# Performance work log

Measured on AMD Instinct MI355X. Metric: run time of the kernel, lower is better.

## Reference

```python
import jax, jax.numpy as jnp
import numpy as np
from jax import lax

W = 50      # window size
EPS = 1e-5  # BatchNorm eps (torch default)


def setup_inputs() -> dict:
    key = jax.random.key(0)
    ks = jax.random.split(key, 40)
    def n(i, shape, s=0.1):
        return (jax.random.normal(ks[i], shape, dtype=jnp.float32) * s).astype(jnp.float32)
    inp = {}
    inp['x'] = jax.random.normal(ks[0], (16, 1, 2048), dtype=jnp.float32)
    # conv stack (eval-mode BatchNorm: running mean/var are params)
    inp['conv1_w'] = n(1, (64, 1, 9));  inp['conv1_b'] = n(2, (64,))
    inp['bn1_g'] = 1.0 + n(3, (64,));   inp['bn1_b'] = n(4, (64,))
    inp['bn1_m'] = n(5, (64,));         inp['bn1_v'] = 0.5 + jax.random.uniform(ks[6], (64,), dtype=jnp.float32)
    inp['conv2_w'] = n(7, (32, 64, 7)); inp['conv2_b'] = n(8, (32,))
    inp['bn2_g'] = 1.0 + n(9, (32,));   inp['bn2_b'] = n(10, (32,))
    inp['bn2_m'] = n(11, (32,));        inp['bn2_v'] = 0.5 + jax.random.uniform(ks[12], (32,), dtype=jnp.float32)
    inp['conv3_w'] = n(13, (16, 32, 5)); inp['conv3_b'] = n(14, (16,))
    inp['bn3_g'] = 1.0 + n(15, (16,));   inp['bn3_b'] = n(16, (16,))
    inp['bn3_m'] = n(17, (16,));         inp['bn3_v'] = 0.5 + jax.random.uniform(ks[18], (16,), dtype=jnp.float32)
    # 2-layer LSTM, hidden 64, input 16 (torch gate order i,f,g,o)
    H = 64
    inp['wih0'] = n(19, (4 * H, 16)); inp['whh0'] = n(20, (4 * H, H))
    inp['bih0'] = n(21, (4 * H,));    inp['bhh0'] = n(22, (4 * H,))
    inp['wih1'] = n(23, (4 * H, H));  inp['whh1'] = n(24, (4 * H, H))
    inp['bih1'] = n(25, (4 * H,));    inp['bhh1'] = n(26, (4 * H,))
    # classifier 64 -> 32 -> 2
    inp['fc1_w'] = n(27, (32, H)); inp['fc1_b'] = n(28, (32,))
    inp['fc2_w'] = n(29, (2, 32)); inp['fc2_b'] = n(30, (2,))
    return inp


def _conv1d(x, w, b, pad):
    # x: [N, Cin, L], w: [Cout, Cin, K]
    y = lax.conv_general_dilated(x, w, (1,), [(pad, pad)],
                                 dimension_numbers=('NCH', 'OIH', 'NCH'))
    return y + b[:, None]


def _bn(x, g, b, m, v):
    # eval-mode BatchNorm1d over channel dim of [N, C, L]
    return (x - m[:, None]) * (g / jnp.sqrt(v + EPS))[:, None] + b[:, None]


def _lstm_layer(x, wih, whh, bih, bhh):
    # x: [B, T, D] -> [B, T, H]; torch gate order (i, f, g, o)
    B, T, D = x.shape
    H = whh.shape[1]
    xs = jnp.transpose(x, (1, 0, 2))                     # [T, B, D]
    pre = xs @ wih.T + (bih + bhh)                       # [T, B, 4H] input projection, hoisted
    def step(carry, p):
        h, c = carry
        g = p + h @ whh.T
        i, f, gg, o = jnp.split(g, 4, axis=-1)
        c = jax.nn.sigmoid(f) * c + jax.nn.sigmoid(i) * jnp.tanh(gg)
        h = jax.nn.sigmoid(o) * jnp.tanh(c)
        return (h, c), h
    h0 = jnp.zeros((B, H), x.dtype)
    _, hs = lax.scan(step, (h0, h0), pre)
    return jnp.transpose(hs, (1, 0, 2))


def reference(x, conv1_w, conv1_b, bn1_g, bn1_b, bn1_m, bn1_v,
              conv2_w, conv2_b, bn2_g, bn2_b, bn2_m, bn2_v,
              conv3_w, conv3_b, bn3_g, bn3_b, bn3_m, bn3_v,
              wih0, whh0, bih0, bhh0, wih1, whh1, bih1, bhh1,
              fc1_w, fc1_b, fc2_w, fc2_b):
    B, C, T = x.shape
    # sliding windows with left zero-pad of W-1 -> [B, T, C, W]
    xp = jnp.pad(x, ((0, 0), (0, 0), (W - 1, 0)))
    idx = jnp.arange(T)[:, None] + jnp.arange(W)[None, :]  # [T, W]
    win = xp[:, :, idx]                                    # [B, C, T, W]
    win = jnp.transpose(win, (0, 2, 1, 3)).reshape(B * T, C, W)
    # conv -> BN(eval) -> ReLU stack (dropout is identity in eval)
    h = jax.nn.relu(_bn(_conv1d(win, conv1_w, conv1_b, 4), bn1_g, bn1_b, bn1_m, bn1_v))
    h = jax.nn.relu(_bn(_conv1d(h, conv2_w, conv2_b, 3), bn2_g, bn2_b, bn2_m, bn2_v))
    h = jax.nn.relu(_bn(_conv1d(h, conv3_w, conv3_b, 2), bn3_g, bn3_b, bn3_m, bn3_v))
    feats = h.mean(axis=-1).reshape(B, T, -1)              # AdaptiveAvgPool1d(1) -> [B, T, 16]
    # 2-layer LSTM
    h1 = _lstm_layer(feats, wih0, whh0, bih0, bhh0)
    h2 = _lstm_layer(h1, wih1, whh1, bih1, bhh1)           # [B, T, 64]
    # classifier
    z = jax.nn.relu(h2 @ fc1_w.T + fc1_b)
    logits = z @ fc2_w.T + fc2_b                           # [B, T, 2]
    return logits
```

## Files before the change

### kernel.cpp

```cpp
#include <hip/hip_runtime.h>

#define EPSV 1e-5f
#define SCOPE_AGENT __HIP_MEMORY_SCOPE_AGENT

__device__ __forceinline__ float fast_rcp(float x) { return __builtin_amdgcn_rcpf(x); }
__device__ __forceinline__ float tanhfast(float x) {
    float e = __expf(2.0f * x);
    return 1.0f - 2.0f * fast_rcp(e + 1.0f);
}
__device__ __forceinline__ float dot4(const float4 w, const float4 v, float a) {
    a = fmaf(w.x, v.x, a);
    a = fmaf(w.y, v.y, a);
    a = fmaf(w.z, v.z, a);
    a = fmaf(w.w, v.w, a);
    return a;
}
#define DPPF(v, ctrl) __int_as_float(__builtin_amdgcn_mov_dpp(__float_as_int(v), (ctrl), 0xF, 0xF, false))

typedef unsigned long long ull;

struct RecS {
    float hbuf[2][80];
    float ring[16][64];
    float xst[16][80];
};
struct EdgeS {
    float A1[64 * 36];
    float A2[32 * 36];
    float xl[16], xr[16];
    float s1[64], t1[64], s2[32], t2[32], s3[16], t3[16];
    float psumE[288];
    float pi[512];
};

__global__ void pack_kernel(const float* __restrict__ w2, const float* __restrict__ w3,
                            float* __restrict__ w2t2, float4* __restrict__ w3p4,
                            float* __restrict__ w3p1, int* __restrict__ sync_ints) {
    int j = blockIdx.x * 256 + threadIdx.x;
    if (j < 16384) {
        int i = j >> 8;
        int o = (j >> 3) & 31;
        int k = j & 7;
        w2t2[j] = (k < 7) ? w2[o * 448 + i * 7 + k] : 0.0f;
    } else if (j < 16896) {
        int e = j - 16384;
        int i = e >> 4, o = e & 15;
        int base = o * 160 + i * 5;
        w3p4[e] = make_float4(w3[base], w3[base + 1], w3[base + 2], w3[base + 3]);
        w3p1[e] = w3[base + 4];
    } else if (j < 16896 + 4096) {
        sync_ints[j - 16896] = 0;
    }
}

__global__ __launch_bounds__(256) void conv1f_kernel(
    const float* __restrict__ x, const float* __restrict__ w1,
    const float* __restrict__ b1, const float* __restrict__ g1,
    const float* __restrict__ be1, const float* __restrict__ m1,
    const float* __restrict__ vv1, float* __restrict__ a1f)
{
    __shared__ float xs[72];
    const int tid = threadIdx.x;
    const int T = blockIdx.x * 64;
    const int b = blockIdx.y;
    if (tid < 72) {
        int gi = T - 49 + tid;
        xs[tid] = (gi >= 0 && gi < 2048) ? x[b * 2048 + gi] : 0.0f;
    }
    const int i = tid & 63, q = tid >> 6;
    float wv[9];
    #pragma unroll
    for (int k = 0; k < 9; ++k) wv[k] = w1[i * 9 + k];
    float sc = g1[i] * rsqrtf(vv1[i] + EPSV);
    float tc = (b1[i] - m1[i]) * sc + be1[i];
    __syncthreads();
    #pragma unroll
    for (int r = 0; r < 16; ++r) {
        int v1 = T + q * 16 + r;
        if (v1 < 2089) {
            float acc = 0.0f;
            #pragma unroll
            for (int k = 0; k < 9; ++k) acc = fmaf(wv[k], xs[q * 16 + r + k], acc);
            a1f[((long)b * 2089 + v1) * 64 + i] = fmaxf(acc * sc + tc, 0.0f);
        }
    }
}

__global__ __launch_bounds__(256) void conv2f_kernel(
    const float* __restrict__ a1f, const float* __restrict__ w2t2,
    const float* __restrict__ b2, const float* __restrict__ g2,
    const float* __restrict__ be2, const float* __restrict__ m2,
    const float* __restrict__ vv2, float* __restrict__ a2f)
{
    __shared__ __align__(16) float As[64 * 104];
    const int tid = threadIdx.x;
    const int T = blockIdx.x * 64;
    const int b = blockIdx.y;
    for (int idx = tid; idx < 1120; idx += 256) {
        int j = idx >> 4, i4 = (idx & 15) * 4;
        int v1 = T + j; if (v1 > 2088) v1 = 2088;
        float4 f = *(const float4*)&a1f[((long)b * 2089 + v1) * 64 + i4];
        int sj = j + ((j >> 3) << 2);
        As[(i4 + 0) * 104 + sj] = f.x;
        As[(i4 + 1) * 104 + sj] = f.y;
        As[(i4 + 2) * 104 + sj] = f.z;
        As[(i4 + 3) * 104 + sj] = f.w;
    }
    const int o = tid >> 3, pg = tid & 7;
    float sc = g2[o] * rsqrtf(vv2[o] + EPSV);
    float tc = (b2[o] - m2[o]) * sc + be2[o];
    __syncthreads();
    float acc[8];
    #pragma unroll
    for (int q = 0; q < 8; ++q) acc[q] = 0.0f;
    for (int i = 0; i < 64; ++i) {
        const float* rowp = &As[i * 104 + 12 * pg];
        float4 A0 = *(const float4*)&rowp[0];
        float4 A1 = *(const float4*)&rowp[4];
        float4 A2 = *(const float4*)&rowp[12];
        float2 A3 = *(const float2*)&rowp[16];
        const float4* wp = (const float4*)&w2t2[(i * 32 + o) * 8];
        float4 Wa = wp[0], Wb = wp[1];
        float av[14] = {A0.x, A0.y, A0.z, A0.w, A1.x, A1.y, A1.z, A1.w,
                        A2.x, A2.y, A2.z, A2.w, A3.x, A3.y};
        float wk[7] = {Wa.x, Wa.y, Wa.z, Wa.w, Wb.x, Wb.y, Wb.z};
        #pragma unroll
        for (int k = 0; k < 7; ++k) {
            #pragma unroll
            for (int q = 0; q < 8; ++q) acc[q] = fmaf(wk[k], av[q + k], acc[q]);
        }
    }
    #pragma unroll
    for (int q = 0; q < 8; ++q) {
        int v2 = T + pg * 8 + q;
        if (v2 < 2083)
            a2f[((long)b * 2083 + v2) * 32 + o] = fmaxf(acc[q] * sc + tc, 0.0f);
    }
}

__global__ __launch_bounds__(256) void conv3f_kernel(
    const float* __restrict__ a2f,
    const float4* __restrict__ w3p4, const float* __restrict__ w3p1,
    const float* __restrict__ b3, const float* __restrict__ g3,
    const float* __restrict__ be3, const float* __restrict__ m3,
    const float* __restrict__ vv3, float* __restrict__ a3f)
{
    __shared__ __align__(16) float A2s[32 * 200];
    const int tid = threadIdx.x;
    const int T = blockIdx.x * 128;
    const int b = blockIdx.y;
    for (int idx = tid; idx < 1056; idx += 256) {
        int j = idx >> 3, i4 = (idx & 7) * 4;
        int v2 = T + j; if (v2 > 2082) v2 = 2082;
        float4 f = *(const float4*)&a2f[((long)b * 2083 + v2) * 32 + i4];
        int sj = j + ((j >> 3) << 2);
        A2s[(i4 + 0) * 200 + sj] = f.x;
        A2s[(i4 + 1) * 200 + sj] = f.y;
        A2s[(i4 + 2) * 200 + sj] = f.z;
        A2s[(i4 + 3) * 200 + sj] = f.w;
    }
    const int o = tid & 15, pg = tid >> 4;
    float sc = g3[o] * rsqrtf(vv3[o] + EPSV);
    float tc = (b3[o] - m3[o]) * sc + be3[o];
    __syncthreads();
    float acc[8];
    #pragma unroll
    for (int q = 0; q < 8; ++q) acc[q] = 0.0f;
    for (int i = 0; i < 32; ++i) {
        const float* rowp = &A2s[i * 200 + 12 * pg];
        float4 R0 = *(const float4*)&rowp[0];
        float4 R1 = *(const float4*)&rowp[4];
        float4 R2 = *(const float4*)&rowp[12];
        float av[12] = {R0.x, R0.y, R0.z, R0.w, R1.x, R1.y, R1.z, R1.w,
                        R2.x, R2.y, R2.z, R2.w};
        float4 wa = w3p4[i * 16 + o];
        float w4 = w3p1[i * 16 + o];
        #pragma unroll
        for (int q = 0; q < 8; ++q) {
            acc[q] = fmaf(wa.x, av[q], acc[q]);
            acc[q] = fmaf(wa.y, av[q + 1], acc[q]);
            acc[q] = fmaf(wa.z, av[q + 2], acc[q]);
            acc[q] = fmaf(wa.w, av[q + 3], acc[q]);
            acc[q] = fmaf(w4,   av[q + 4], acc[q]);
        }
    }
    #pragma unroll
    for (int q = 0; q < 8; ++q) {
        int v3 = T + pg * 8 + q;
        if (v3 < 2079)
            a3f[((long)b * 2080 + v3) * 16 + o] = fmaxf(acc[q] * sc + tc, 0.0f);
        else if (v3 < 2080)
            a3f[((long)b * 2080 + v3) * 16 + o] = 0.0f;
    }
}

__device__ __forceinline__ void rec0_body(char* smemraw, int b,
    const float* __restrict__ feats,
    const float* __restrict__ wih, const float* __restrict__ whh,
    const float* __restrict__ bih, const float* __restrict__ bhh,
    float* __restrict__ hout, int* __restrict__ cnt0, int* __restrict__ flag1)
{
    RecS* s = (RecS*)smemraw;
    const int tid = threadIdx.x;
    const int j = tid >> 2, kq = tid & 3;
    __builtin_amdgcn_s_setprio(1);

    const float4* pa = (const float4*)(whh + (0 * 64 + j) * 64 + kq * 16);
    const float4* pb = (const float4*)(whh + (1 * 64 + j) * 64 + kq * 16);
    const float4* pc_ = (const float4*)(whh + (2 * 64 + j) * 64 + kq * 16);
    const float4* pd = (const float4*)(whh + (3 * 64 + j) * 64 + kq * 16);
    float4 A0 = pa[0], A1 = pa[1], A2 = pa[2], A3 = pa[3];
    float4 B0 = pb[0], B1 = pb[1], B2 = pb[2], B3 = pb[3];
    float4 C0 = pc_[0], C1 = pc_[1], C2 = pc_[2], C3 = pc_[3];
    float4 D0 = pd[0], D1 = pd[1], D2 = pd[2], D3 = pd[3];
    float4 xw0 = *(const float4*)(wih + (0 * 64 + j) * 16 + kq * 4);
    float4 xw1 = *(const float4*)(wih + (1 * 64 + j) * 16 + kq * 4);
    float4 xw2 = *(const float4*)(wih + (2 * 64 + j) * 16 + kq * 4);
    float4 xw3 = *(const float4*)(wih + (3 * 64 + j) * 16 + kq * 4);
    const float bb0 = bih[j] + bhh[j];
    const float bb1 = bih[64 + j] + bhh[64 + j];
    const float bb2 = bih[128 + j] + bhh[128 + j];
    const float bb3 = bih[192 + j] + bhh[192 + j];

    if (tid < 64) s->hbuf[1][(tid >> 4) * 20 + (tid & 15)] = 0.0f;
    float cst = 0.0f;
    const float* fbase = feats + (long)b * 32768;
    __syncthreads();

#define STEP0(k) { \
        const float4* hp_ = (const float4*)&s->hbuf[((k) + 1) & 1][kq * 20]; \
        float4 h0_ = hp_[0], h1_ = hp_[1], h2_ = hp_[2], h3_ = hp_[3]; \
        float4 xv_ = *(const float4*)&s->xst[(k)][kq * 4]; \
        float p0 = dot4(A3, h3_, dot4(A2, h2_, dot4(A1, h1_, dot4(A0, h0_, dot4(xw0, xv_, 0.f))))); \
        float p1 = dot4(B3, h3_, dot4(B2, h2_, dot4(B1, h1_, dot4(B0, h0_, dot4(xw1, xv_, 0.f))))); \
        float p2 = dot4(C3, h3_, dot4(C2, h2_, dot4(C1, h1_, dot4(C0, h0_, dot4(xw2, xv_, 0.f))))); \
        float p3 = dot4(D3, h3_, dot4(D2, h2_, dot4(D1, h1_, dot4(D0, h0_, dot4(xw3, xv_, 0.f))))); \
        p0 += DPPF(p0, 0xB1); p1 += DPPF(p1, 0xB1); p2 += DPPF(p2, 0xB1); p3 += DPPF(p3, 0xB1); \
        p0 += DPPF(p0, 0x4E); p1 += DPPF(p1, 0x4E); p2 += DPPF(p2, 0x4E); p3 += DPPF(p3, 0x4E); \
        float gi = 1.0f - fast_rcp(__expf(p0 + bb0) + 1.0f); \
        float gf = 1.0f - fast_rcp(__expf(p1 + bb1) + 1.0f); \
        float gg = 1.0f - 2.0f * fast_rcp(__expf(2.0f * (p2 + bb2)) + 1.0f); \
        float go = 1.0f - fast_rcp(__expf(p3 + bb3) + 1.0f); \
        cst = fmaf(gf, cst, gi * gg); \
        float h_ = go * tanhfast(cst); \
        if (kq == 0) { s->hbuf[(k) & 1][(j >> 4) * 20 + (j & 15)] = h_; s->ring[(k)][j] = h_; } \
        __syncthreads(); \
    }

    for (int c = 0; c < 128; ++c) {
        if (tid == 0) {
            while (__hip_atomic_load(&cnt0[b * 128 + c], __ATOMIC_RELAXED, SCOPE_AGENT) < 16)
                __builtin_amdgcn_s_sleep(2);
        }
        __syncthreads();
        s->xst[tid >> 4][tid & 15] =
            __hip_atomic_load(fbase + c * 256 + tid, __ATOMIC_RELAXED, SCOPE_AGENT);
        __syncthreads();
        STEP0(0)  STEP0(1)  STEP0(2)  STEP0(3)
        STEP0(4)  STEP0(5)  STEP0(6)  STEP0(7)
        STEP0(8)  STEP0(9)  STEP0(10) STEP0(11)
        STEP0(12) STEP0(13) STEP0(14) STEP0(15)
        {
            ull* dst = (ull*)(hout + ((long)b * 2048 + c * 16) * 64);
            ull v0 = ((const ull*)s->ring)[tid];
            ull v1 = ((const ull*)s->ring)[tid + 256];
            __hip_atomic_store(dst + tid, v0, __ATOMIC_RELAXED, SCOPE_AGENT);
            __hip_atomic_store(dst + tid + 256, v1, __ATOMIC_RELAXED, SCOPE_AGENT);
            __syncthreads();
            if (tid == 0)
                __hip_atomic_store(&flag1[b * 128 + c], 1, __ATOMIC_RELAXED, SCOPE_AGENT);
        }
    }
#undef STEP0
}

__device__ __forceinline__ void rec1_body(char* smemraw, int b,
    const float* __restrict__ h1o,
    const float* __restrict__ wih, const float* __restrict__ whh,
    const float* __restrict__ bih, const float* __restrict__ bhh,
    float* __restrict__ hout, int* __restrict__ flag1)
{
    RecS* s = (RecS*)smemraw;
    const int tid = threadIdx.x;
    const int j = tid >> 2, kq = tid & 3;
    __builtin_amdgcn_s_setprio(1);

    const float4* pa = (const float4*)(whh + (0 * 64 + j) * 64 + kq * 16);
    const float4* pb = (const float4*)(whh + (1 * 64 + j) * 64 + kq * 16);
    const float4* pc_ = (const float4*)(whh + (2 * 64 + j) * 64 + kq * 16);
    const float4* pd = (const float4*)(whh + (3 * 64 + j) * 64 + kq * 16);
    float4 A0 = pa[0], A1 = pa[1], A2 = pa[2], A3 = pa[3];
    float4 B0 = pb[0], B1 = pb[1], B2 = pb[2], B3 = pb[3];
    float4 C0 = pc_[0], C1 = pc_[1], C2 = pc_[2], C3 = pc_[3];
    float4 D0 = pd[0], D1 = pd[1], D2 = pd[2], D3 = pd[3];
    const float4* qa = (const float4*)(wih + (0 * 64 + j) * 64 + kq * 16);
    const float4* qb = (const float4*)(wih + (1 * 64 + j) * 64 + kq * 16);
    const float4* qc = (const float4*)(wih + (2 * 64 + j) * 64 + kq * 16);
    const float4* qd = (const float4*)(wih + (3 * 64 + j) * 64 + kq * 16);
    float4 XA0 = qa[0], XA1 = qa[1], XA2 = qa[2], XA3 = qa[3];
    float4 XB0 = qb[0], XB1 = qb[1], XB2 = qb[2], XB3 = qb[3];
    float4 XC0 = qc[0], XC1 = qc[1], XC2 = qc[2], XC3 = qc[3];
    float4 XD0 = qd[0], XD1 = qd[1], XD2 = qd[2], XD3 = qd[3];
    const float bb0 = bih[j] + bhh[j];
    const float bb1 = bih[64 + j] + bhh[64 + j];
    const float bb2 = bih[128 + j] + bhh[128 + j];
    const float bb3 = bih[192 + j] + bhh[192 + j];

    if (tid < 64) s->hbuf[1][(tid >> 4) * 20 + (tid & 15)] = 0.0f;
    float cst = 0.0f;
    __syncthreads();

#define STEP1(k) { \
        const float4* hp_ = (const float4*)&s->hbuf[((k) + 1) & 1][kq * 20]; \
        float4 h0_ = hp_[0], h1_ = hp_[1], h2_ = hp_[2], h3_ = hp_[3]; \
        const float4* xp_ = (const float4*)&s->xst[(k)][kq * 20]; \
        float4 x0_ = xp_[0], x1_ = xp_[1], x2_ = xp_[2], x3_ = xp_[3]; \
        float p0 = dot4(A3, h3_, dot4(A2, h2_, dot4(A1, h1_, dot4(A0, h0_, \
                   dot4(XA3, x3_, dot4(XA2, x2_, dot4(XA1, x1_, dot4(XA0, x0_, 0.f)))))))); \
        float p1 = dot4(B3, h3_, dot4(B2, h2_, dot4(B1, h1_, dot4(B0, h0_, \
                   dot4(XB3, x3_, dot4(XB2, x2_, dot4(XB1, x1_, dot4(XB0, x0_, 0.f)))))))); \
        float p2 = dot4(C3, h3_, dot4(C2, h2_, dot4(C1, h1_, dot4(C0, h0_, \
                   dot4(XC3, x3_, dot4(XC2, x2_, dot4(XC1, x1_, dot4(XC0, x0_, 0.f)))))))); \
        float p3 = dot4(D3, h3_, dot4(D2, h2_, dot4(D1, h1_, dot4(D0, h0_, \
                   dot4(XD3, x3_, dot4(XD2, x2_, dot4(XD1, x1_, dot4(XD0, x0_, 0.f)))))))); \
        p0 += DPPF(p0, 0xB1); p1 += DPPF(p1, 0xB1); p2 += DPPF(p2, 0xB1); p3 += DPPF(p3, 0xB1); \
        p0 += DPPF(p0, 0x4E); p1 += DPPF(p1, 0x4E); p2 += DPPF(p2, 0x4E); p3 += DPPF(p3, 0x4E); \
        float gi = 1.0f - fast_rcp(__expf(p0 + bb0) + 1.0f); \
        float gf = 1.0f - fast_rcp(__expf(p1 + bb1) + 1.0f); \
        float gg = 1.0f - 2.0f * fast_rcp(__expf(2.0f * (p2 + bb2)) + 1.0f); \
        float go = 1.0f - fast_rcp(__expf(p3 + bb3) + 1.0f); \
        cst = fmaf(gf, cst, gi * gg); \
        float h_ = go * tanhfast(cst); \
        if (kq == 0) { s->hbuf[(k) & 1][(j >> 4) * 20 + (j & 15)] = h_; s->ring[(k)][j] = h_; } \
        __syncthreads(); \
    }

    for (int c = 0; c < 128; ++c) {
        if (tid == 0) {
            while (__hip_atomic_load(&flag1[b * 128 + c], __ATOMIC_RELAXED, SCOPE_AGENT) < 1)
                __builtin_amdgcn_s_sleep(2);
        }
        __syncthreads();
        {
            const ull* src = (const ull*)(h1o + ((long)b * 2048 + c * 16) * 64);
            ull v0 = __hip_atomic_load(src + tid, __ATOMIC_RELAXED, SCOPE_AGENT);
            ull v1 = __hip_atomic_load(src + tid + 256, __ATOMIC_RELAXED, SCOPE_AGENT);
            int u0 = tid, u1 = tid + 256;
            int k0 = u0 >> 5, p0i = (u0 & 31) * 2;
            int k1 = u1 >> 5, p1i = (u1 & 31) * 2;
            *(ull*)&s->xst[k0][(p0i >> 4) * 20 + (p0i & 15)] = v0;
            *(ull*)&s->xst[k1][(p1i >> 4) * 20 + (p1i & 15)] = v1;
        }
        __syncthreads();
        STEP1(0)  STEP1(1)  STEP1(2)  STEP1(3)
        STEP1(4)  STEP1(5)  STEP1(6)  STEP1(7)
        STEP1(8)  STEP1(9)  STEP1(10) STEP1(11)
        STEP1(12) STEP1(13) STEP1(14) STEP1(15)
        {
            float4* dst = (float4*)(hout + ((long)b * 2048 + c * 16) * 64);
            dst[tid] = ((const float4*)s->ring)[tid];
        }
    }
#undef STEP1
}

__device__ void edge_worker(char* smemraw, int w,
    const float* __restrict__ x,
    const float* __restrict__ w1,
    const float* __restrict__ b1, const float* __restrict__ g1,
    const float* __restrict__ be1, const float* __restrict__ m1, const float* __restrict__ vv1,
    const float* __restrict__ b2, const float* __restrict__ g2,
    const float* __restrict__ be2, const float* __restrict__ m2, const float* __restrict__ vv2,
    const float* __restrict__ b3, const float* __restrict__ g3,
    const float* __restrict__ be3, const float* __restrict__ m3, const float* __restrict__ vv3,
    const float* __restrict__ w2t2,
    const float4* __restrict__ w3p4, const float* __restrict__ w3p1,
    const float* __restrict__ a1f, const float* __restrict__ a2f,
    const float* __restrict__ a3f,
    float* __restrict__ feats, int* __restrict__ cnt0)
{
    EdgeS* s = (EdgeS*)smemraw;
    const int tid = threadIdx.x;

    for (int idx = tid; idx < 1088; idx += 256) {
        if (idx < 768) {
            int row = idx / 12, z = idx - row * 12;
            int slot = (z < 3) ? z : (z < 6 ? 10 + z : 20 + z);
            s->A1[row * 36 + slot] = 0.0f;
        } else {
            int e = idx - 768;
            int row = e / 10, z = e - row * 10;
            int slot = (z < 2) ? z : (z < 5 ? 11 + z : 22 + z);
            s->A2[row * 36 + slot] = 0.0f;
        }
    }
    if (tid < 64) {
        float sc = g1[tid] * rsqrtf(vv1[tid] + EPSV);
        s->s1[tid] = sc;
        s->t1[tid] = (b1[tid] - m1[tid]) * sc + be1[tid];
    } else if (tid < 96) {
        int o = tid - 64;
        float sc = g2[o] * rsqrtf(vv2[o] + EPSV);
        s->s2[o] = sc;
        s->t2[o] = (b2[o] - m2[o]) * sc + be2[o];
    } else if (tid < 112) {
        int o = tid - 96;
        float sc = g3[o] * rsqrtf(vv3[o] + EPSV);
        s->s3[o] = sc;
        s->t3[o] = (b3[o] - m3[o]) * sc + be3[o];
    }
    const int o1 = tid >> 2, g1q = tid & 3;
    float wv[9];
    #pragma unroll
    for (int k = 0; k < 9; ++k) wv[k] = w1[o1 * 9 + k];
    __syncthreads();
    const float sc1 = s->s1[o1], tc1 = s->t1[o1];

    for (int tile = w; tile < 32768; tile += 448) {
        const int b = tile & 15, t = tile >> 4;

        if (tid < 128) {
            int dv = tid >> 2, o4 = (tid & 3) * 4;
            *(float4*)&s->pi[dv * 16 + o4] =
                *(const float4*)&a3f[((long)b * 2080 + t + dv) * 16 + o4];
        }
        if (tid >= 112 && tid < 128) {
            int m = tid - 112;
            float v = 0.0f;
            if (m >= 4) { int gi = t - 53 + m; if (gi >= 0) v = x[b * 2048 + gi]; }
            s->xl[m] = v;
        } else if (tid >= 128 && tid < 144) {
            int m = tid - 128;
            float v = 0.0f;
            if (m <= 7) { int gi = t - 7 + m; if (gi >= 0) v = x[b * 2048 + gi]; }
            s->xr[m] = v;
        }
        {
            if (tid < 96) {
                int d = tid >> 4, i4 = (tid & 15) * 4;
                float4 f = *(const float4*)&a1f[((long)b * 2089 + t + d) * 64 + i4];
                int slot = 7 + d;
                s->A1[(i4 + 0) * 36 + slot] = f.x;
                s->A1[(i4 + 1) * 36 + slot] = f.y;
                s->A1[(i4 + 2) * 36 + slot] = f.z;
                s->A1[(i4 + 3) * 36 + slot] = f.w;
            } else if (tid < 192) {
                int e = tid - 96;
                int d = e >> 4, i4 = (e & 15) * 4;
                float4 f = *(const float4*)&a1f[((long)b * 2089 + t + 36 + d) * 64 + i4];
                int slot = 16 + d;
                s->A1[(i4 + 0) * 36 + slot] = f.x;
                s->A1[(i4 + 1) * 36 + slot] = f.y;
                s->A1[(i4 + 2) * 36 + slot] = f.z;
                s->A1[(i4 + 3) * 36 + slot] = f.w;
            } else if (tid < 224) {
                int e = tid - 192;
                int d = e >> 3, i4 = (e & 7) * 4;
                float4 f = *(const float4*)&a2f[((long)b * 2083 + t + d) * 32 + i4];
                int slot = 9 + d;
                s->A2[(i4 + 0) * 36 + slot] = f.x;
                s->A2[(i4 + 1) * 36 + slot] = f.y;
                s->A2[(i4 + 2) * 36 + slot] = f.z;
                s->A2[(i4 + 3) * 36 + slot] = f.w;
            } else {
                int e = tid - 224;
                int d = e >> 3, i4 = (e & 7) * 4;
                float4 f = *(const float4*)&a2f[((long)b * 2083 + t + 32 + d) * 32 + i4];
                int slot = 16 + d;
                s->A2[(i4 + 0) * 36 + slot] = f.x;
                s->A2[(i4 + 1) * 36 + slot] = f.y;
                s->A2[(i4 + 2) * 36 + slot] = f.z;
                s->A2[(i4 + 3) * 36 + slot] = f.w;
            }
        }
        __syncthreads();

        {
            float accL = 0.0f, accR = 0.0f;
            #pragma unroll
            for (int k = 0; k < 9; ++k) {
                accL = fmaf(wv[k], s->xl[g1q + k], accL);
                accR = fmaf(wv[k], s->xr[g1q + k], accR);
            }
            s->A1[o1 * 36 + 3 + g1q]  = fmaxf(accL * sc1 + tc1, 0.0f);
            s->A1[o1 * 36 + 22 + g1q] = fmaxf(accR * sc1 + tc1, 0.0f);
        }
        __syncthreads();

        {
            const int o = tid >> 3, side = (tid >> 2) & 1, isub = tid & 3;
            const int sbase = side * 16;
            float acc[7];
            #pragma unroll
            for (int q = 0; q < 7; ++q) acc[q] = 0.0f;
            #pragma unroll 2
            for (int ii = 0; ii < 16; ++ii) {
                int i = 4 * ii + isub;
                const float* rp = &s->A1[i * 36 + sbase];
                float4 R0 = *(const float4*)&rp[0];
                float4 R1 = *(const float4*)&rp[4];
                float4 R2 = *(const float4*)&rp[8];
                float r12 = rp[12];
                float av[13] = {R0.x, R0.y, R0.z, R0.w, R1.x, R1.y, R1.z, R1.w,
                                R2.x, R2.y, R2.z, R2.w, r12};
                const float4* wp = (const float4*)&w2t2[(i * 32 + o) * 8];
                float4 Wa = wp[0], Wb = wp[1];
                float wk[7] = {Wa.x, Wa.y, Wa.z, Wa.w, Wb.x, Wb.y, Wb.z};
                #pragma unroll
                for (int k = 0; k < 7; ++k) {
                    #pragma unroll
                    for (int q = 0; q < 7; ++q) acc[q] = fmaf(wk[k], av[q + k], acc[q]);
                }
            }
            #pragma unroll
            for (int q = 0; q < 7; ++q) {
                acc[q] += DPPF(acc[q], 0xB1);
                acc[q] += DPPF(acc[q], 0x4E);
            }
            if (isub == 0) {
                float sc = s->s2[o], tc = s->t2[o];
                #pragma unroll
                for (int q = 0; q < 7; ++q) {
                    float r = fmaxf(acc[q] * sc + tc, 0.0f);
                    s->A2[o * 36 + (side ? 20 + q : 2 + q)] = r;
                }
            }
        }
        __syncthreads();

        {
            const int o = (tid >> 2) & 15, isub = tid & 3;
            const int side = (tid >> 6) & 1, pg = tid >> 7;
            float acc[5];
            #pragma unroll
            for (int n = 0; n < 5; ++n) acc[n] = 0.0f;
            if (pg == 0) {
                #pragma unroll 2
                for (int ii = 0; ii < 8; ++ii) {
                    int i = 4 * ii + isub;
                    const float* rp = &s->A2[i * 36 + side * 16];
                    float4 R0 = *(const float4*)&rp[0];
                    float4 R1 = *(const float4*)&rp[4];
                    float t8 = rp[8];
                    float av[9] = {R0.x, R0.y, R0.z, R0.w, R1.x, R1.y, R1.z, R1.w, t8};
                    float4 wa = w3p4[i * 16 + o];
                    float w4 = w3p1[i * 16 + o];
                    #pragma unroll
                    for (int n = 0; n < 5; ++n) {
                        acc[n] = fmaf(wa.x, av[n], acc[n]);
                        acc[n] = fmaf(wa.y, av[n + 1], acc[n]);
                        acc[n] = fmaf(wa.z, av[n + 2], acc[n]);
                        acc[n] = fmaf(wa.w, av[n + 3], acc[n]);
                        acc[n] = fmaf(w4,   av[n + 4], acc[n]);
                    }
                }
            } else {
                #pragma unroll 2
                for (int ii = 0; ii < 8; ++ii) {
                    int i = 4 * ii + isub;
                    const float* rp = &s->A2[i * 36 + side * 16];
                    float4 R1 = *(const float4*)&rp[4];
                    float4 R2 = *(const float4*)&rp[8];
                    float t12 = rp[12];
                    float av[8] = {R1.y, R1.z, R1.w, R2.x, R2.y, R2.z, R2.w, t12};
                    float4 wa = w3p4[i * 16 + o];
                    float w4 = w3p1[i * 16 + o];
                    #pragma unroll
                    for (int n = 0; n < 4; ++n) {
                        acc[n] = fmaf(wa.x, av[n], acc[n]);
                        acc[n] = fmaf(wa.y, av[n + 1], acc[n]);
                        acc[n] = fmaf(wa.z, av[n + 2], acc[n]);
                        acc[n] = fmaf(wa.w, av[n + 3], acc[n]);
                        acc[n] = fmaf(w4,   av[n + 4], acc[n]);
                    }
                }
            }
            #pragma unroll
            for (int n = 0; n < 5; ++n) {
                acc[n] += DPPF(acc[n], 0xB1);
                acc[n] += DPPF(acc[n], 0x4E);
            }
            if (isub == 0) {
                float sc = s->s3[o], tc = s->t3[o];
                if (pg == 0) {
                    #pragma unroll
                    for (int n = 0; n < 5; ++n)
                        s->psumE[(side * 9 + n) * 16 + o] = fmaxf(acc[n] * sc + tc, 0.0f);
                } else {
                    #pragma unroll
                    for (int n = 0; n < 4; ++n)
                        s->psumE[(side * 9 + 5 + n) * 16 + o] = fmaxf(acc[n] * sc + tc, 0.0f);
                }
            }
        }
        __syncthreads();

        if (tid < 16) {
            float e = 0.0f;
            #pragma unroll
            for (int P3 = 0; P3 < 18; ++P3) e += s->psumE[P3 * 16 + tid];
            float ii = 0.0f;
            #pragma unroll
            for (int dv = 0; dv < 32; ++dv) ii += s->pi[dv * 16 + tid];
            __hip_atomic_store(&feats[((long)b * 2048 + t) * 16 + tid], (e + ii) * (1.0f / 50.0f),
                               __ATOMIC_RELAXED, SCOPE_AGENT);
        }
        __syncthreads();
        if (tid == 0)
            __hip_atomic_fetch_add(&cnt0[b * 128 + (t >> 4)], 1, __ATOMIC_RELAXED, SCOPE_AGENT);
    }
}

__global__ __launch_bounds__(256, 2) void fused_kernel(
    const float* __restrict__ x,
    const float* __restrict__ w1, const float* __restrict__ b1,
    const float* __restrict__ g1, const float* __restrict__ be1,
    const float* __restrict__ m1, const float* __restrict__ vv1,
    const float* __restrict__ b2,
    const float* __restrict__ g2, const float* __restrict__ be2,
    const float* __restrict__ m2, const float* __restrict__ vv2,
    const float* __restrict__ b3,
    const float* __restrict__ g3, const float* __restrict__ be3,
    const float* __restrict__ m3, const float* __restrict__ vv3,
    const float* __restrict__ w2t2,
    const float4* __restrict__ w3p4, const float* __restrict__ w3p1,
    const float* __restrict__ a1f, const float* __restrict__ a2f,
    const float* __restrict__ a3f,
    const float* __restrict__ wih0, const float* __restrict__ whh0,
    const float* __restrict__ bih0, const float* __restrict__ bhh0,
    const float* __restrict__ wih1, const float* __restrict__ whh1,
    const float* __restrict__ bih1, const float* __restrict__ bhh1,
    float* __restrict__ feats, float* __restrict__ h1o, float* __restrict__ h2o,
    int* __restrict__ cnt0, int* __restrict__ flag1)
{
    __shared__ __align__(16) char smem[sizeof(EdgeS) > sizeof(RecS) ? sizeof(EdgeS) : sizeof(RecS)];

    const int bid = blockIdx.x;
    if (bid < 16) { rec0_body(smem, bid, feats, wih0, whh0, bih0, bhh0, h1o, cnt0, flag1); return; }
    if (bid < 32) { rec1_body(smem, bid - 16, h1o, wih1, whh1, bih1, bhh1, h2o, flag1); return; }
    if (bid >= 256 && bid < 288) return;

    int w = (bid < 256) ? (bid - 32) : (bid - 288 + 224);
    edge_worker(smem, w, x, w1, b1, g1, be1, m1, vv1, b2, g2, be2, m2, vv2,
                b3, g3, be3, m3, vv3, w2t2, w3p4, w3p1, a1f, a2f, a3f, feats, cnt0);
}

__global__ __launch_bounds__(256) void fc_kernel(
    const float* __restrict__ h2o,
    const float* __restrict__ fc1w, const float* __restrict__ fc1b,
    const float* __restrict__ fc2w, const float* __restrict__ fc2b,
    float* __restrict__ out)
{
    int r = blockIdx.x * 256 + threadIdx.x;
    float h[64];
    const float4* hp = (const float4*)(h2o + (long)r * 64);
    #pragma unroll
    for (int i = 0; i < 16; ++i) {
        float4 v = hp[i];
        h[4 * i] = v.x; h[4 * i + 1] = v.y; h[4 * i + 2] = v.z; h[4 * i + 3] = v.w;
    }
    float l0 = fc2b[0], l1 = fc2b[1];
    #pragma unroll 4
    for (int j = 0; j < 32; ++j) {
        float z = fc1b[j];
        #pragma unroll
        for (int k = 0; k < 64; ++k) z = fmaf(h[k], fc1w[j * 64 + k], z);
        z = fmaxf(z, 0.0f);
        l0 = fmaf(z, fc2w[j], l0);
        l1 = fmaf(z, fc2w[32 + j], l1);
    }
    out[r * 2] = l0;
    out[r * 2 + 1] = l1;
}

extern "C" void kernel_launch(void* const* d_in, const int* in_sizes, int n_in,
                              void* d_out, int out_size, void* d_ws, size_t ws_size,
                              hipStream_t stream) {
    const float* x    = (const float*)d_in[0];
    const float* w1   = (const float*)d_in[1];
    const float* b1   = (const float*)d_in[2];
    const float* g1   = (const float*)d_in[3];
    const float* be1  = (const float*)d_in[4];
    const float* m1   = (const float*)d_in[5];
    const float* v1   = (const float*)d_in[6];
    const float* w2   = (const float*)d_in[7];
    const float* b2   = (const float*)d_in[8];
    const float* g2   = (const float*)d_in[9];
    const float* be2  = (const float*)d_in[10];
    const float* m2   = (const float*)d_in[11];
    const float* v2   = (const float*)d_in[12];
    const float* w3   = (const float*)d_in[13];
    const float* b3   = (const float*)d_in[14];
    const float* g3   = (const float*)d_in[15];
    const float* be3  = (const float*)d_in[16];
    const float* m3   = (const float*)d_in[17];
    const float* v3   = (const float*)d_in[18];
    const float* wih0 = (const float*)d_in[19];
    const float* whh0 = (const float*)d_in[20];
    const float* bih0 = (const float*)d_in[21];
    const float* bhh0 = (const float*)d_in[22];
    const float* wih1 = (const float*)d_in[23];
    const float* whh1 = (const float*)d_in[24];
    const float* bih1 = (const float*)d_in[25];
    const float* bhh1 = (const float*)d_in[26];
    const float* fc1w = (const float*)d_in[27];
    const float* fc1b = (const float*)d_in[28];
    const float* fc2w = (const float*)d_in[29];
    const float* fc2b = (const float*)d_in[30];
    float* out = (float*)d_out;

    float* ws    = (float*)d_ws;
    float* feats = ws;
    float* h2o   = feats + 32768 * 16;
    float* w2t2  = h2o + 32768 * 64;
    float* w3p4f = w2t2 + 16384;
    float* w3p1  = w3p4f + 2048;
    float* h1o   = w3p1 + 512;
    float* a1f   = h1o + 32768 * 64;
    float* a2f   = a1f + 16 * 2089 * 64;
    float* a3f   = a2f + 16 * 2083 * 32;
    int*   cnt0  = (int*)(a3f + 16 * 2080 * 16);
    int*   flag1 = cnt0 + 2048;

    hipLaunchKernelGGL(pack_kernel, dim3(82), dim3(256), 0, stream,
                       w2, w3, w2t2, (float4*)w3p4f, w3p1, cnt0);
    hipLaunchKernelGGL(conv1f_kernel, dim3(33, 16), dim3(256), 0, stream,
                       x, w1, b1, g1, be1, m1, v1, a1f);
    hipLaunchKernelGGL(conv2f_kernel, dim3(33, 16), dim3(256), 0, stream,
                       a1f, w2t2, b2, g2, be2, m2, v2, a2f);
    hipLaunchKernelGGL(conv3f_kernel, dim3(17, 16), dim3(256), 0, stream,
                       a2f, (const float4*)w3p4f, w3p1, b3, g3, be3, m3, v3, a3f);
    hipLaunchKernelGGL(fused_kernel, dim3(512), dim3(256), 0, stream,
                       x, w1, b1, g1, be1, m1, v1, b2, g2, be2, m2, v2,
                       b3, g3, be3, m3, v3, w2t2, (const float4*)w3p4f, w3p1,
                       a1f, a2f, a3f,
                       wih0, whh0, bih0, bhh0, wih1, whh1, bih1, bhh1,
                       feats, h1o, h2o, cnt0, flag1);
    hipLaunchKernelGGL(fc_kernel, dim3(128), dim3(256), 0, stream,
                       h2o, fc1w, fc1b, fc2w, fc2b, out);
}
```

Measured before the change: 1.195 ms.

## Merge both LSTM layers into one 512-thread block with skewed layer pipelining

Layer 0 and layer 1 recurrences for each batch item now run in a single 512-thread block: each half handles one layer, and layer 1 runs one step behind layer 0, reading layer 0's hidden state directly from shared memory. This removes the global h1o round trip and the flag1 inter-block handshake on the serial critical path. Edge workers are also doubled up to two 256-thread halves per block, each with its own shared-memory slice, processing interleaved tiles with an active guard. In exchange, every step's barrier now spans 512 threads, and the divergent half-paths may raise register pressure.

```diff
diff --git a/kernel.cpp b/kernel.cpp
--- a/kernel.cpp
+++ b/kernel.cpp
@@ -19,9 +19,9 @@
 
 typedef unsigned long long ull;
 
-struct RecS {
-    float hbuf[2][80];
-    float ring[16][64];
+struct Rec2S {
+    float hbuf0[2][80];
+    float hbuf1[2][80];
     float xst[16][80];
 };
 struct EdgeS {
@@ -194,17 +194,24 @@
     }
 }
 
-__device__ __forceinline__ void rec0_body(char* smemraw, int b,
+__device__ void rec_merged(char* smemraw, int b,
     const float* __restrict__ feats,
-    const float* __restrict__ wih, const float* __restrict__ whh,
-    const float* __restrict__ bih, const float* __restrict__ bhh,
-    float* __restrict__ hout, int* __restrict__ cnt0, int* __restrict__ flag1)
+    const float* __restrict__ wih0, const float* __restrict__ whh0,
+    const float* __restrict__ bih0, const float* __restrict__ bhh0,
+    const float* __restrict__ wih1, const float* __restrict__ whh1,
+    const float* __restrict__ bih1, const float* __restrict__ bhh1,
+    float* __restrict__ h2o, int* __restrict__ cnt0)
 {
-    RecS* s = (RecS*)smemraw;
+    Rec2S* s = (Rec2S*)smemraw;
     const int tid = threadIdx.x;
-    const int j = tid >> 2, kq = tid & 3;
+    const int half = tid >> 8;
+    const int lt = tid & 255;
+    const int j = lt >> 2, kq = lt & 3;
     __builtin_amdgcn_s_setprio(1);
 
+    const float* whh = half ? whh1 : whh0;
+    const float* bih = half ? bih1 : bih0;
+    const float* bhh = half ? bhh1 : bhh0;
     const float4* pa = (const float4*)(whh + (0 * 64 + j) * 64 + kq * 16);
     const float4* pb = (const float4*)(whh + (1 * 64 + j) * 64 + kq * 16);
     const float4* pc_ = (const float4*)(whh + (2 * 64 + j) * 64 + kq * 16);
@@ -213,24 +220,46 @@
     float4 B0 = pb[0], B1 = pb[1], B2 = pb[2], B3 = pb[3];
     float4 C0 = pc_[0], C1 = pc_[1], C2 = pc_[2], C3 = pc_[3];
     float4 D0 = pd[0], D1 = pd[1], D2 = pd[2], D3 = pd[3];
-    float4 xw0 = *(const float4*)(wih + (0 * 64 + j) * 16 + kq * 4);
-    float4 xw1 = *(const float4*)(wih + (1 * 64 + j) * 16 + kq * 4);
-    float4 xw2 = *(const float4*)(wih + (2 * 64 + j) * 16 + kq * 4);
-    float4 xw3 = *(const float4*)(wih + (3 * 64 + j) * 16 + kq * 4);
     const float bb0 = bih[j] + bhh[j];
     const float bb1 = bih[64 + j] + bhh[64 + j];
     const float bb2 = bih[128 + j] + bhh[128 + j];
     const float bb3 = bih[192 + j] + bhh[192 + j];
 
-    if (tid < 64) s->hbuf[1][(tid >> 4) * 20 + (tid & 15)] = 0.0f;
+    float4 z4 = make_float4(0.f, 0.f, 0.f, 0.f);
+    float4 XA0 = z4, XA1 = z4, XA2 = z4, XA3 = z4;
+    float4 XB0 = z4, XB1 = z4, XB2 = z4, XB3 = z4;
+    float4 XC0 = z4, XC1 = z4, XC2 = z4, XC3 = z4;
+    float4 XD0 = z4, XD1 = z4, XD2 = z4, XD3 = z4;
+    float4 xw0 = z4, xw1 = z4, xw2 = z4, xw3 = z4;
+    if (half) {
+        const float4* qa = (const float4*)(wih1 + (0 * 64 + j) * 64 + kq * 16);
+        const float4* qb = (const float4*)(wih1 + (1 * 64 + j) * 64 + kq * 16);
+        const float4* qc = (const float4*)(wih1 + (2 * 64 + j) * 64 + kq * 16);
+        const float4* qd = (const float4*)(wih1 + (3 * 64 + j) * 64 + kq * 16);
+        XA0 = qa[0]; XA1 = qa[1]; XA2 = qa[2]; XA3 = qa[3];
+        XB0 = qb[0]; XB1 = qb[1]; XB2 = qb[2]; XB3 = qb[3];
+        XC0 = qc[0]; XC1 = qc[1]; XC2 = qc[2]; XC3 = qc[3];
+        XD0 = qd[0]; XD1 = qd[1]; XD2 = qd[2]; XD3 = qd[3];
+    } else {
+        xw0 = *(const float4*)(wih0 + (0 * 64 + j) * 16 + kq * 4);
+        xw1 = *(const float4*)(wih0 + (1 * 64 + j) * 16 + kq * 4);
+        xw2 = *(const float4*)(wih0 + (2 * 64 + j) * 16 + kq * 4);
+        xw3 = *(const float4*)(wih0 + (3 * 64 + j) * 16 + kq * 4);
+    }
+
+    if (lt < 64) {
+        if (half == 0) s->hbuf0[1][(lt >> 4) * 20 + (lt & 15)] = 0.0f;
+        else           s->hbuf1[1][(lt >> 4) * 20 + (lt & 15)] = 0.0f;
+    }
     float cst = 0.0f;
     const float* fbase = feats + (long)b * 32768;
     __syncthreads();
 
-#define STEP0(k) { \
-        const float4* hp_ = (const float4*)&s->hbuf[((k) + 1) & 1][kq * 20]; \
+#define LSTEP0(kk) \
+    if (half == 0) { \
+        const float4* hp_ = (const float4*)&s->hbuf0[((kk) + 1) & 1][kq * 20]; \
         float4 h0_ = hp_[0], h1_ = hp_[1], h2_ = hp_[2], h3_ = hp_[3]; \
-        float4 xv_ = *(const float4*)&s->xst[(k)][kq * 4]; \
+        float4 xv_ = *(const float4*)&s->xst[(kk)][kq * 4]; \
         float p0 = dot4(A3, h3_, dot4(A2, h2_, dot4(A1, h1_, dot4(A0, h0_, dot4(xw0, xv_, 0.f))))); \
         float p1 = dot4(B3, h3_, dot4(B2, h2_, dot4(B1, h1_, dot4(B0, h0_, dot4(xw1, xv_, 0.f))))); \
         float p2 = dot4(C3, h3_, dot4(C2, h2_, dot4(C1, h1_, dot4(C0, h0_, dot4(xw2, xv_, 0.f))))); \
@@ -243,77 +272,14 @@
         float go = 1.0f - fast_rcp(__expf(p3 + bb3) + 1.0f); \
         cst = fmaf(gf, cst, gi * gg); \
         float h_ = go * tanhfast(cst); \
-        if (kq == 0) { s->hbuf[(k) & 1][(j >> 4) * 20 + (j & 15)] = h_; s->ring[(k)][j] = h_; } \
-        __syncthreads(); \
-    }
-
-    for (int c = 0; c < 128; ++c) {
-        if (tid == 0) {
-            while (__hip_atomic_load(&cnt0[b * 128 + c], __ATOMIC_RELAXED, SCOPE_AGENT) < 16)
-                __builtin_amdgcn_s_sleep(2);
-        }
-        __syncthreads();
-        s->xst[tid >> 4][tid & 15] =
-            __hip_atomic_load(fbase + c * 256 + tid, __ATOMIC_RELAXED, SCOPE_AGENT);
-        __syncthreads();
-        STEP0(0)  STEP0(1)  STEP0(2)  STEP0(3)
-        STEP0(4)  STEP0(5)  STEP0(6)  STEP0(7)
-        STEP0(8)  STEP0(9)  STEP0(10) STEP0(11)
-        STEP0(12) STEP0(13) STEP0(14) STEP0(15)
-        {
-            ull* dst = (ull*)(hout + ((long)b * 2048 + c * 16) * 64);
-            ull v0 = ((const ull*)s->ring)[tid];
-            ull v1 = ((const ull*)s->ring)[tid + 256];
-            __hip_atomic_store(dst + tid, v0, __ATOMIC_RELAXED, SCOPE_AGENT);
-            __hip_atomic_store(dst + tid + 256, v1, __ATOMIC_RELAXED, SCOPE_AGENT);
-            __syncthreads();
-            if (tid == 0)
-                __hip_atomic_store(&flag1[b * 128 + c], 1, __ATOMIC_RELAXED, SCOPE_AGENT);
-        }
-    }
-#undef STEP0
-}
-
-__device__ __forceinline__ void rec1_body(char* smemraw, int b,
-    const float* __restrict__ h1o,
-    const float* __restrict__ wih, const float* __restrict__ whh,
-    const float* __restrict__ bih, const float* __restrict__ bhh,
-    float* __restrict__ hout, int* __restrict__ flag1)
-{
-    RecS* s = (RecS*)smemraw;
-    const int tid = threadIdx.x;
-    const int j = tid >> 2, kq = tid & 3;
-    __builtin_amdgcn_s_setprio(1);
-
-    const float4* pa = (const float4*)(whh + (0 * 64 + j) * 64 + kq * 16);
-    const float4* pb = (const float4*)(whh + (1 * 64 + j) * 64 + kq * 16);
-    const float4* pc_ = (const float4*)(whh + (2 * 64 + j) * 64 + kq * 16);
-    const float4* pd = (const float4*)(whh + (3 * 64 + j) * 64 + kq * 16);
-    float4 A0 = pa[0], A1 = pa[1], A2 = pa[2], A3 = pa[3];
-    float4 B0 = pb[0], B1 = pb[1], B2 = pb[2], B3 = pb[3];
-    float4 C0 = pc_[0], C1 = pc_[1], C2 = pc_[2], C3 = pc_[3];
-    float4 D0 = pd[0], D1 = pd[1], D2 = pd[2], D3 = pd[3];
-    const float4* qa = (const float4*)(wih + (0 * 64 + j) * 64 + kq * 16);
-    const float4* qb = (const float4*)(wih + (1 * 64 + j) * 64 + kq * 16);
-    const float4* qc = (const float4*)(wih + (2 * 64 + j) * 64 + kq * 16);
-    const float4* qd = (const float4*)(wih + (3 * 64 + j) * 64 + kq * 16);
-    float4 XA0 = qa[0], XA1 = qa[1], XA2 = qa[2], XA3 = qa[3];
-    float4 XB0 = qb[0], XB1 = qb[1], XB2 = qb[2], XB3 = qb[3];
-    float4 XC0 = qc[0], XC1 = qc[1], XC2 = qc[2], XC3 = qc[3];
-    float4 XD0 = qd[0], XD1 = qd[1], XD2 = qd[2], XD3 = qd[3];
-    const float bb0 = bih[j] + bhh[j];
-    const float bb1 = bih[64 + j] + bhh[64 + j];
-    const float bb2 = bih[128 + j] + bhh[128 + j];
-    const float bb3 = bih[192 + j] + bhh[192 + j];
-
-    if (tid < 64) s->hbuf[1][(tid >> 4) * 20 + (tid & 15)] = 0.0f;
-    float cst = 0.0f;
-    __syncthreads();
-
-#define STEP1(k) { \
-        const float4* hp_ = (const float4*)&s->hbuf[((k) + 1) & 1][kq * 20]; \
+        if (kq == 0) s->hbuf0[(kk) & 1][(j >> 4) * 20 + (j & 15)] = h_; \
+    }
+
+#define LSTEP1(mval, P) \
+    if (half == 1 && (mval) >= 0) { \
+        const float4* hp_ = (const float4*)&s->hbuf1[(P) ^ 1][kq * 20]; \
         float4 h0_ = hp_[0], h1_ = hp_[1], h2_ = hp_[2], h3_ = hp_[3]; \
-        const float4* xp_ = (const float4*)&s->xst[(k)][kq * 20]; \
+        const float4* xp_ = (const float4*)&s->hbuf0[(P)][kq * 20]; \
         float4 x0_ = xp_[0], x1_ = xp_[1], x2_ = xp_[2], x3_ = xp_[3]; \
         float p0 = dot4(A3, h3_, dot4(A2, h2_, dot4(A1, h1_, dot4(A0, h0_, \
                    dot4(XA3, x3_, dot4(XA2, x2_, dot4(XA1, x1_, dot4(XA0, x0_, 0.f)))))))); \
@@ -331,40 +297,47 @@
         float go = 1.0f - fast_rcp(__expf(p3 + bb3) + 1.0f); \
         cst = fmaf(gf, cst, gi * gg); \
         float h_ = go * tanhfast(cst); \
-        if (kq == 0) { s->hbuf[(k) & 1][(j >> 4) * 20 + (j & 15)] = h_; s->ring[(k)][j] = h_; } \
-        __syncthreads(); \
+        if (kq == 0) { \
+            s->hbuf1[(P)][(j >> 4) * 20 + (j & 15)] = h_; \
+            h2o[((long)b * 2048 + (mval)) * 64 + j] = h_; \
+        } \
     }
 
     for (int c = 0; c < 128; ++c) {
+        const int gb = c * 16;
         if (tid == 0) {
-            while (__hip_atomic_load(&flag1[b * 128 + c], __ATOMIC_RELAXED, SCOPE_AGENT) < 1)
+            while (__hip_atomic_load(&cnt0[b * 128 + c], __ATOMIC_RELAXED, SCOPE_AGENT) < 16)
                 __builtin_amdgcn_s_sleep(2);
         }
         __syncthreads();
-        {
-            const ull* src = (const ull*)(h1o + ((long)b * 2048 + c * 16) * 64);
-            ull v0 = __hip_atomic_load(src + tid, __ATOMIC_RELAXED, SCOPE_AGENT);
-            ull v1 = __hip_atomic_load(src + tid + 256, __ATOMIC_RELAXED, SCOPE_AGENT);
-            int u0 = tid, u1 = tid + 256;
-            int k0 = u0 >> 5, p0i = (u0 & 31) * 2;
-            int k1 = u1 >> 5, p1i = (u1 & 31) * 2;
-            *(ull*)&s->xst[k0][(p0i >> 4) * 20 + (p0i & 15)] = v0;
-            *(ull*)&s->xst[k1][(p1i >> 4) * 20 + (p1i & 15)] = v1;
-        }
+        if (half == 0)
+            s->xst[lt >> 4][lt & 15] =
+                __hip_atomic_load(fbase + c * 256 + lt, __ATOMIC_RELAXED, SCOPE_AGENT);
+        LSTEP1(gb - 1, 1)
         __syncthreads();
-        STEP1(0)  STEP1(1)  STEP1(2)  STEP1(3)
-        STEP1(4)  STEP1(5)  STEP1(6)  STEP1(7)
-        STEP1(8)  STEP1(9)  STEP1(10) STEP1(11)
-        STEP1(12) STEP1(13) STEP1(14) STEP1(15)
-        {
-            float4* dst = (float4*)(hout + ((long)b * 2048 + c * 16) * 64);
-            dst[tid] = ((const float4*)s->ring)[tid];
-        }
-    }
-#undef STEP1
-}
-
-__device__ void edge_worker(char* smemraw, int w,
+        LSTEP0(0)                       __syncthreads();
+        LSTEP0(1)   LSTEP1(gb + 0, 0)  __syncthreads();
+        LSTEP0(2)   LSTEP1(gb + 1, 1)  __syncthreads();
+        LSTEP0(3)   LSTEP1(gb + 2, 0)  __syncthreads();
+        LSTEP0(4)   LSTEP1(gb + 3, 1)  __syncthreads();
+        LSTEP0(5)   LSTEP1(gb + 4, 0)  __syncthreads();
+        LSTEP0(6)   LSTEP1(gb + 5, 1)  __syncthreads();
+        LSTEP0(7)   LSTEP1(gb + 6, 0)  __syncthreads();
+        LSTEP0(8)   LSTEP1(gb + 7, 1)  __syncthreads();
+        LSTEP0(9)   LSTEP1(gb + 8, 0)  __syncthreads();
+        LSTEP0(10)  LSTEP1(gb + 9, 1)  __syncthreads();
+        LSTEP0(11)  LSTEP1(gb + 10, 0) __syncthreads();
+        LSTEP0(12)  LSTEP1(gb + 11, 1) __syncthreads();
+        LSTEP0(13)  LSTEP1(gb + 12, 0) __syncthreads();
+        LSTEP0(14)  LSTEP1(gb + 13, 1) __syncthreads();
+        LSTEP0(15)  LSTEP1(gb + 14, 0) __syncthreads();
+    }
+    LSTEP1(2047, 1)
+#undef LSTEP0
+#undef LSTEP1
+}
+
+__device__ void edge_worker2(char* smemraw, int w,
     const float* __restrict__ x,
     const float* __restrict__ w1,
     const float* __restrict__ b1, const float* __restrict__ g1,
@@ -379,8 +352,9 @@
     const float* __restrict__ a3f,
     float* __restrict__ feats, int* __restrict__ cnt0)
 {
-    EdgeS* s = (EdgeS*)smemraw;
-    const int tid = threadIdx.x;
+    const int half = threadIdx.x >> 8;
+    EdgeS* s = ((EdgeS*)smemraw) + half;
+    const int tid = threadIdx.x & 255;
 
     for (int idx = tid; idx < 1088; idx += 256) {
         if (idx < 768) {
@@ -416,8 +390,11 @@
     __syncthreads();
     const float sc1 = s->s1[o1], tc1 = s->t1[o1];
 
-    for (int tile = w; tile < 32768; tile += 448) {
-        const int b = tile & 15, t = tile >> 4;
+    for (int it = 0; it < 69; ++it) {
+        int tile = it * 480 + 2 * w + half;
+        bool active = tile < 32768;
+        int tt = active ? tile : 32767;
+        const int b = tt & 15, t = tt >> 4;
 
         if (tid < 128) {
             int dv = tid >> 2, o4 = (tid & 3) * 4;
@@ -595,7 +572,7 @@
         }
         __syncthreads();
 
-        if (tid < 16) {
+        if (tid < 16 && active) {
             float e = 0.0f;
             #pragma unroll
             for (int P3 = 0; P3 < 18; ++P3) e += s->psumE[P3 * 16 + tid];
@@ -606,12 +583,12 @@
                                __ATOMIC_RELAXED, SCOPE_AGENT);
         }
         __syncthreads();
-        if (tid == 0)
+        if (tid == 0 && active)
             __hip_atomic_fetch_add(&cnt0[b * 128 + (t >> 4)], 1, __ATOMIC_RELAXED, SCOPE_AGENT);
     }
 }
 
-__global__ __launch_bounds__(256, 2) void fused_kernel(
+__global__ __launch_bounds__(512, 2) void fused_kernel(
     const float* __restrict__ x,
     const float* __restrict__ w1, const float* __restrict__ b1,
     const float* __restrict__ g1, const float* __restrict__ be1,
@@ -630,19 +607,19 @@
     const float* __restrict__ bih0, const float* __restrict__ bhh0,
     const float* __restrict__ wih1, const float* __restrict__ whh1,
     const float* __restrict__ bih1, const float* __restrict__ bhh1,
-    float* __restrict__ feats, float* __restrict__ h1o, float* __restrict__ h2o,
-    int* __restrict__ cnt0, int* __restrict__ flag1)
+    float* __restrict__ feats, float* __restrict__ h2o,
+    int* __restrict__ cnt0)
 {
-    __shared__ __align__(16) char smem[sizeof(EdgeS) > sizeof(RecS) ? sizeof(EdgeS) : sizeof(RecS)];
+    __shared__ __align__(16) char smem[sizeof(EdgeS) * 2 > sizeof(Rec2S) ? sizeof(EdgeS) * 2 : sizeof(Rec2S)];
 
     const int bid = blockIdx.x;
-    if (bid < 16) { rec0_body(smem, bid, feats, wih0, whh0, bih0, bhh0, h1o, cnt0, flag1); return; }
-    if (bid < 32) { rec1_body(smem, bid - 16, h1o, wih1, whh1, bih1, bhh1, h2o, flag1); return; }
-    if (bid >= 256 && bid < 288) return;
-
-    int w = (bid < 256) ? (bid - 32) : (bid - 288 + 224);
-    edge_worker(smem, w, x, w1, b1, g1, be1, m1, vv1, b2, g2, be2, m2, vv2,
-                b3, g3, be3, m3, vv3, w2t2, w3p4, w3p1, a1f, a2f, a3f, feats, cnt0);
+    if (bid < 16) {
+        rec_merged(smem, bid, feats, wih0, whh0, bih0, bhh0,
+                   wih1, whh1, bih1, bhh1, h2o, cnt0);
+        return;
+    }
+    edge_worker2(smem, bid - 16, x, w1, b1, g1, be1, m1, vv1, b2, g2, be2, m2, vv2,
+                 b3, g3, be3, m3, vv3, w2t2, w3p4, w3p1, a1f, a2f, a3f, feats, cnt0);
 }
 
 __global__ __launch_bounds__(256) void fc_kernel(
@@ -720,7 +697,7 @@
     float* a2f   = a1f + 16 * 2089 * 64;
     float* a3f   = a2f + 16 * 2083 * 32;
     int*   cnt0  = (int*)(a3f + 16 * 2080 * 16);
-    int*   flag1 = cnt0 + 2048;
+    (void)in_sizes; (void)n_in; (void)out_size; (void)ws_size;
 
     hipLaunchKernelGGL(pack_kernel, dim3(82), dim3(256), 0, stream,
                        w2, w3, w2t2, (float4*)w3p4f, w3p1, cnt0);
@@ -730,12 +707,12 @@
                        a1f, w2t2, b2, g2, be2, m2, v2, a2f);
     hipLaunchKernelGGL(conv3f_kernel, dim3(17, 16), dim3(256), 0, stream,
                        a2f, (const float4*)w3p4f, w3p1, b3, g3, be3, m3, v3, a3f);
-    hipLaunchKernelGGL(fused_kernel, dim3(512), dim3(256), 0, stream,
+    hipLaunchKernelGGL(fused_kernel, dim3(256), dim3(512), 0, stream,
                        x, w1, b1, g1, be1, m1, v1, b2, g2, be2, m2, v2,
                        b3, g3, be3, m3, v3, w2t2, (const float4*)w3p4f, w3p1,
                        a1f, a2f, a3f,
                        wih0, whh0, bih0, bhh0, wih1, whh1, bih1, bhh1,
-                       feats, h1o, h2o, cnt0, flag1);
+                       feats, h2o, cnt0);
     hipLaunchKernelGGL(fc_kernel, dim3(128), dim3(256), 0, stream,
                        h2o, fc1w, fc1b, fc2w, fc2b, out);
 }
```

Measured after the change: 1.312 ms. +9.8%, slower.
